# Performance work log

Measured on AMD Instinct MI355X. Metric: run time of the kernel, lower is better.

Reference implementation:

```python
import jax, jax.numpy as jnp
import numpy as np

B, D, H = 16384, 1024, 8
DH = D // H
LN_EPS = 1e-5


def setup_inputs() -> dict:
    key = jax.random.key(0)
    ks = jax.random.split(key, 16)
    s = 0.02  # weight init scale to keep softmax logits sane
    d = {}
    d['f40'] = jax.random.normal(ks[0], (B, D), jnp.float32)
    d['f100'] = jax.random.normal(ks[1], (B, D), jnp.float32)
    d['f200'] = jax.random.normal(ks[2], (B, D), jnp.float32)
    d['f400'] = jax.random.normal(ks[3], (B, D), jnp.float32)
    d['mag_emb'] = jax.random.normal(ks[4], (4, D), jnp.float32)
    i = 5
    for mag in ('100', '200', '400'):
        d[f'in_w_{mag}'] = jax.random.normal(ks[i], (3 * D, D), jnp.float32) * s
        d[f'in_b_{mag}'] = jnp.zeros((3 * D,), jnp.float32)
        d[f'out_w_{mag}'] = jax.random.normal(ks[i + 1], (D, D), jnp.float32) * s
        d[f'out_b_{mag}'] = jnp.zeros((D,), jnp.float32)
        d[f'ln_w_{mag}'] = jnp.ones((D,), jnp.float32)
        d[f'ln_b_{mag}'] = jnp.zeros((D,), jnp.float32)
        i += 2
    return d


def _layer_norm(x, w, b):
    m = jnp.mean(x, axis=-1, keepdims=True)
    v = jnp.mean(jnp.square(x - m), axis=-1, keepdims=True)
    return (x - m) * jax.lax.rsqrt(v + LN_EPS) * w + b


def _mha(q, kv, in_w, in_b, out_w, out_b):
    # q: [B,1,D], kv: [B,S,D]. Matches torch nn.MultiheadAttention (batch_first).
    S = kv.shape[1]
    wq, wk, wv = jnp.split(in_w, 3, axis=0)
    bq, bk, bv = jnp.split(in_b, 3)
    qp = (q @ wq.T + bq).reshape(B, 1, H, DH)
    kp = (kv @ wk.T + bk).reshape(B, S, H, DH)
    vp = (kv @ wv.T + bv).reshape(B, S, H, DH)
    scores = jnp.einsum('bqhd,bkhd->bhqk', qp, kp) / np.sqrt(DH).astype(np.float32)
    attn = jax.nn.softmax(scores, axis=-1)           # [B,H,1,S]
    out = jnp.einsum('bhqk,bkhd->bqhd', attn, vp).reshape(B, 1, D)
    out = (out @ out_w.T + out_b)[:, 0, :]           # [B,D]
    return out, attn.mean(axis=1)                     # weights averaged over heads: [B,1,S]


def reference(f40, f100, f200, f400, mag_emb,
              in_w_100, in_b_100, out_w_100, out_b_100, ln_w_100, ln_b_100,
              in_w_200, in_b_200, out_w_200, out_b_200, ln_w_200, ln_b_200,
              in_w_400, in_b_400, out_w_400, out_b_400, ln_w_400, ln_b_400):
    feats = (f40, f100, f200, f400)
    enh = [f + mag_emb[i] for i, f in enumerate(feats)]
    level_params = [
        (in_w_100, in_b_100, out_w_100, out_b_100, ln_w_100, ln_b_100),
        (in_w_200, in_b_200, out_w_200, out_b_200, ln_w_200, ln_b_200),
        (in_w_400, in_b_400, out_w_400, out_b_400, ln_w_400, ln_b_400),
    ]
    hier = [enh[0]]
    attn_maps = []
    for i, (iw, ib, ow, ob, lw, lb) in enumerate(level_params):
        ctx = jnp.stack(hier, axis=1)                 # [B, i+1, D]
        attended, w = _mha(enh[i + 1][:, None, :], ctx, iw, ib, ow, ob)
        fused = _layer_norm(enh[i + 1] + attended, lw, lb)
        hier.append(fused)
        attn_maps.append(w)
    return (hier[0], hier[1], hier[2], hier[3], attn_maps[0], attn_maps[1], attn_maps[2])
```

## Files before the change

### kernel.cpp

```cpp
#include <hip/hip_runtime.h>

typedef unsigned short u16;
typedef unsigned int u32;

#define NB 16384
#define ND 1024
static constexpr size_t BD = (size_t)NB * ND;
static constexpr size_t DD = (size_t)ND * ND;

typedef __attribute__((ext_vector_type(8))) short s16x8;
typedef __attribute__((ext_vector_type(4))) float f32x4;

__device__ __forceinline__ u16 f2bf(float f) {
  union { float f; u32 u; } v; v.f = f;
  return (u16)((v.u + 0x7fffu + ((v.u >> 16) & 1u)) >> 16);
}
__device__ __forceinline__ float asf(u32 u) {
  union { u32 u; float f; } v; v.u = u; return v.f;
}
__device__ __forceinline__ uint2 pack4(float a, float b, float c, float d) {
  uint2 p;
  p.x = (u32)f2bf(a) | ((u32)f2bf(b) << 16);
  p.y = (u32)f2bf(c) | ((u32)f2bf(d) << 16);
  return p;
}
__device__ __forceinline__ void load16bf(const u16* p, float* o) {
  const uint4* q = (const uint4*)p;
  uint4 u0 = q[0], u1 = q[1];
  u32 w[8] = {u0.x, u0.y, u0.z, u0.w, u1.x, u1.y, u1.z, u1.w};
#pragma unroll
  for (int i = 0; i < 8; ++i) {
    o[2 * i]     = asf(w[i] << 16);
    o[2 * i + 1] = asf(w[i] & 0xffff0000u);
  }
}
__device__ __forceinline__ void store16bf(u16* p, const float* o) {
  uint4 u0, u1;
  u0.x = (u32)f2bf(o[0])  | ((u32)f2bf(o[1])  << 16);
  u0.y = (u32)f2bf(o[2])  | ((u32)f2bf(o[3])  << 16);
  u0.z = (u32)f2bf(o[4])  | ((u32)f2bf(o[5])  << 16);
  u0.w = (u32)f2bf(o[6])  | ((u32)f2bf(o[7])  << 16);
  u1.x = (u32)f2bf(o[8])  | ((u32)f2bf(o[9])  << 16);
  u1.y = (u32)f2bf(o[10]) | ((u32)f2bf(o[11]) << 16);
  u1.z = (u32)f2bf(o[12]) | ((u32)f2bf(o[13]) << 16);
  u1.w = (u32)f2bf(o[14]) | ((u32)f2bf(o[15]) << 16);
  ((uint4*)p)[0] = u0;
  ((uint4*)p)[1] = u1;
}

#define G2L(gp, lp) __builtin_amdgcn_global_load_lds( \
    (__attribute__((address_space(1))) void*)(void*)(gp), \
    (__attribute__((address_space(3))) void*)(lp), 16, 0, 0)

template<int BF16_OUT>
__device__ __forceinline__ void gemm_core(
    const u16* __restrict__ A, const u16* __restrict__ Bm,
    const float* __restrict__ bias, void* __restrict__ Cp,
    int N, int K, int ldc, int row0, int col0)
{
  __shared__ __align__(16) u16 lA[128 * 64];
  __shared__ __align__(16) u16 lB[128 * 64];
  const int tid  = threadIdx.x;
  const int wave = tid >> 6;
  const int lane = tid & 63;
  const int wm = (wave >> 1) * 64;
  const int wn = (wave & 1) * 64;
  const int fr = lane & 15;
  const int fq = lane >> 4;
  const int srow = tid >> 3;
  const int scol = ((tid & 7) ^ (srow & 7)) * 8;

  f32x4 acc[4][4];
#pragma unroll
  for (int i = 0; i < 4; ++i)
#pragma unroll
    for (int j = 0; j < 4; ++j) acc[i][j] = (f32x4){0.f, 0.f, 0.f, 0.f};

  const u16* Abase = A  + (size_t)(row0 + srow) * K + scol;
  const u16* Bbase = Bm + (size_t)(col0 + srow) * K + scol;
  u16* lAw = lA + wave * 512;
  u16* lBw = lB + wave * 512;
  const int rsw = (fr & 7) << 3;

  for (int kt = 0; kt < K; kt += 64) {
#pragma unroll
    for (int c = 0; c < 4; ++c) {
      G2L(Abase + (size_t)(c * 32) * K + kt, lAw + c * 2048);
      G2L(Bbase + (size_t)(c * 32) * K + kt, lBw + c * 2048);
    }
    __syncthreads();

#pragma unroll
    for (int kk = 0; kk < 2; ++kk) {
      s16x8 af[4], bfr[4];
#pragma unroll
      for (int i = 0; i < 4; ++i) {
        af[i]  = *(const s16x8*)&lA[(wm + i * 16 + fr) * 64 + ((kk * 32 + fq * 8) ^ rsw)];
        bfr[i] = *(const s16x8*)&lB[(wn + i * 16 + fr) * 64 + ((kk * 32 + fq * 8) ^ rsw)];
      }
#pragma unroll
      for (int i = 0; i < 4; ++i)
#pragma unroll
        for (int j = 0; j < 4; ++j)
          acc[i][j] = __builtin_amdgcn_mfma_f32_16x16x32_bf16(af[i], bfr[j], acc[i][j], 0, 0, 0);
    }
    __syncthreads();
  }

#pragma unroll
  for (int i = 0; i < 4; ++i) {
#pragma unroll
    for (int j = 0; j < 4; ++j) {
      const int col = col0 + wn + j * 16 + fr;
      const float bb = bias ? bias[col] : 0.f;
#pragma unroll
      for (int r = 0; r < 4; ++r) {
        const int row = row0 + wm + i * 16 + fq * 4 + r;
        const float v = acc[i][j][r] + bb;
        if (BF16_OUT) ((u16*)Cp)[(size_t)row * ldc + col] = f2bf(v);
        else          ((float*)Cp)[(size_t)row * ldc + col] = v;
      }
    }
  }
}

__device__ __forceinline__ void swz_rowcol(int* row0, int* col0) {
  const int nwg = gridDim.x * gridDim.y;
  int wgid = blockIdx.y * gridDim.x + blockIdx.x;
  wgid = (wgid & 7) * (nwg >> 3) + (wgid >> 3);
  *row0 = (wgid / gridDim.x) * 128;
  *col0 = (wgid % gridDim.x) * 128;
}

template<int BF16_OUT>
__global__ __launch_bounds__(256, 3) void gemm_bt(
    const u16* __restrict__ A, const u16* __restrict__ Bm,
    const float* __restrict__ bias, void* __restrict__ Cp,
    int N, int K, int ldc)
{
  int row0, col0;
  swz_rowcol(&row0, &col0);
  gemm_core<BF16_OUT>(A, Bm, bias, Cp, N, K, ldc, row0, col0);
}

struct Ptr3 { const u16* a0; const u16* a1; const u16* a2;
              u16* c0; u16* c1; u16* c2; };

__global__ __launch_bounds__(256, 3) void kv_gemm(
    Ptr3 p, const u16* __restrict__ Bm, int K)
{
  int row0, col0;
  swz_rowcol(&row0, &col0);
  const u16* A; u16* C;
  if (blockIdx.z == 0)      { A = p.a0; C = p.c0; }
  else if (blockIdx.z == 1) { A = p.a1; C = p.c1; }
  else                      { A = p.a2; C = p.c2; }
  gemm_core<1>(A, Bm, nullptr, C, 2048, K, 2048, row0, col0);
}

__global__ __launch_bounds__(256) void prep_k(
    const float* __restrict__ f40, const float* __restrict__ f200,
    const float* __restrict__ f400, const float* __restrict__ mag,
    float* __restrict__ out0, u16* __restrict__ h0b,
    u16* __restrict__ e2b, u16* __restrict__ e3b)
{
  const size_t j = ((size_t)blockIdx.x * 256 + threadIdx.x) * 4;
  const int d = (int)(j & 1023);
  float4 m0 = *(const float4*)(mag + d);
  float4 m2 = *(const float4*)(mag + 2 * ND + d);
  float4 m3 = *(const float4*)(mag + 3 * ND + d);
  float4 a  = *(const float4*)(f40 + j);
  float4 c2 = *(const float4*)(f200 + j);
  float4 c3 = *(const float4*)(f400 + j);
  float4 h0;
  h0.x = a.x + m0.x; h0.y = a.y + m0.y; h0.z = a.z + m0.z; h0.w = a.w + m0.w;
  *(float4*)(out0 + j) = h0;
  *(uint2*)(h0b + j) = pack4(h0.x, h0.y, h0.z, h0.w);
  *(uint2*)(e2b + j) = pack4(c2.x + m2.x, c2.y + m2.y, c2.z + m2.z, c2.w + m2.w);
  *(uint2*)(e3b + j) = pack4(c3.x + m3.x, c3.y + m3.y, c3.z + m3.z, c3.w + m3.w);
}

__global__ __launch_bounds__(256) void ones_k(float* __restrict__ p) {
  p[blockIdx.x * 256 + threadIdx.x] = 1.0f;
}

__global__ __launch_bounds__(256) void convw_k(
    const float* __restrict__ iw, const float* __restrict__ ow,
    u16* __restrict__ wbf)
{
  const size_t j = ((size_t)blockIdx.x * 256 + threadIdx.x) * 4;
  const size_t IW = (size_t)3 * ND * ND;
  const float* src = (j < IW) ? (iw + j) : (ow + (j - IW));
  float4 v = *(const float4*)src;
  *(uint2*)(wbf + j) = pack4(v.x, v.y, v.z, v.w);
}

__global__ __launch_bounds__(256) void transpose_bf_k(
    const float* __restrict__ src, u16* __restrict__ dst)
{
  __shared__ float t[32][33];
  const int bx = blockIdx.x & 31, by = blockIdx.x >> 5;
  const int tx = threadIdx.x & 31, ty = threadIdx.x >> 5;
#pragma unroll
  for (int r = 0; r < 4; ++r)
    t[ty + r * 8][tx] = src[(size_t)(by * 32 + ty + r * 8) * ND + bx * 32 + tx];
  __syncthreads();
#pragma unroll
  for (int r = 0; r < 4; ++r)
    dst[(size_t)(bx * 32 + ty + r * 8) * ND + by * 32 + tx] = f2bf(t[tx][ty + r * 8]);
}

__global__ __launch_bounds__(256) void biasfold_k(
    const float* __restrict__ bv, const float* __restrict__ wo,
    const float* __restrict__ bo, float* __restrict__ c0)
{
  const int i = blockIdx.x;
  float s = 0.f;
  for (int k = threadIdx.x; k < ND; k += 256) s += bv[k] * wo[(size_t)i * ND + k];
#pragma unroll
  for (int m = 1; m <= 32; m <<= 1) s += __shfl_xor(s, m, 64);
  __shared__ float red[4];
  const int wv = threadIdx.x >> 6, ln = threadIdx.x & 63;
  if (ln == 0) red[wv] = s;
  __syncthreads();
  if (threadIdx.x == 0) c0[i] = bo[i] + red[0] + red[1] + red[2] + red[3];
}

template<int S>
__global__ __launch_bounds__(256) void attn_k(
    const u16* __restrict__ qp, const u16* __restrict__ kva,
    const u16* __restrict__ kvb, const u16* __restrict__ kvc,
    u16* __restrict__ att, float* __restrict__ amap)
{
  const int wave = threadIdx.x >> 6, lane = threadIdx.x & 63;
  const int b = blockIdx.x * 4 + wave;
  const int d0 = lane * 16;
  const u16* kv[3] = {kva, kvb, kvc};

  float q[16];
  load16bf(qp + (size_t)b * ND + d0, q);

  float sc[S];
  float mx = -1e30f;
#pragma unroll
  for (int s = 0; s < S; ++s) {
    float k[16];
    load16bf(kv[s] + (size_t)b * 2 * ND + d0, k);
    float dot = 0.f;
#pragma unroll
    for (int i = 0; i < 16; ++i) dot += q[i] * k[i];
    dot += __shfl_xor(dot, 1, 64);
    dot += __shfl_xor(dot, 2, 64);
    dot += __shfl_xor(dot, 4, 64);
    sc[s] = dot * 0.08838834764831845f;
    mx = fmaxf(mx, sc[s]);
  }
  float w_[S];
  float den = 0.f;
#pragma unroll
  for (int s = 0; s < S; ++s) { w_[s] = __expf(sc[s] - mx); den += w_[s]; }
  const float inv = 1.f / den;

  float o[16] = {0.f, 0.f, 0.f, 0.f, 0.f, 0.f, 0.f, 0.f,
                 0.f, 0.f, 0.f, 0.f, 0.f, 0.f, 0.f, 0.f};
#pragma unroll
  for (int s = 0; s < S; ++s) {
    float v[16];
    load16bf(kv[s] + (size_t)b * 2 * ND + ND + d0, v);
    const float ws = w_[s] * inv;
#pragma unroll
    for (int i = 0; i < 16; ++i) o[i] += ws * v[i];
  }
  store16bf(att + (size_t)b * ND + d0, o);

#pragma unroll
  for (int s = 0; s < S; ++s) {
    float t = w_[s] * inv;
    t += __shfl_xor(t, 8, 64);
    t += __shfl_xor(t, 16, 64);
    t += __shfl_xor(t, 32, 64);
    if (lane == 0) amap[(size_t)b * S + s] = t * 0.125f;
  }
}

__global__ __launch_bounds__(256) void ln_k(
    const float* __restrict__ f, const float* __restrict__ emb,
    const u16* __restrict__ ob, const float* __restrict__ lw,
    const float* __restrict__ lb, float* __restrict__ outp,
    u16* __restrict__ hbf)
{
  const int b = blockIdx.x, t = threadIdx.x;
  const int d = t * 4;
  const size_t off = (size_t)b * ND + d;
  float4 xf = *(const float4*)(f + off);
  float4 ef = *(const float4*)(emb + d);
  uint2 ov  = *(const uint2*)(ob + off);
  float o0 = asf(ov.x << 16), o1 = asf(ov.x & 0xffff0000u);
  float o2 = asf(ov.y << 16), o3 = asf(ov.y & 0xffff0000u);
  float x0 = xf.x + ef.x + o0;
  float x1 = xf.y + ef.y + o1;
  float x2 = xf.z + ef.z + o2;
  float x3 = xf.w + ef.w + o3;
  float s  = x0 + x1 + x2 + x3;
  float s2 = x0 * x0 + x1 * x1 + x2 * x2 + x3 * x3;
#pragma unroll
  for (int m = 1; m <= 32; m <<= 1) {
    s  += __shfl_xor(s,  m, 64);
    s2 += __shfl_xor(s2, m, 64);
  }
  __shared__ float red[8];
  const int wv = t >> 6, ln = t & 63;
  if (ln == 0) { red[wv] = s; red[4 + wv] = s2; }
  __syncthreads();
  s  = red[0] + red[1] + red[2] + red[3];
  s2 = red[4] + red[5] + red[6] + red[7];
  const float mean = s * (1.f / 1024.f);
  const float var  = s2 * (1.f / 1024.f) - mean * mean;
  const float r = rsqrtf(var + 1e-5f);
  float4 w4 = *(const float4*)(lw + d);
  float4 b4 = *(const float4*)(lb + d);
  float4 y;
  y.x = (x0 - mean) * r * w4.x + b4.x;
  y.y = (x1 - mean) * r * w4.y + b4.y;
  y.z = (x2 - mean) * r * w4.z + b4.z;
  y.w = (x3 - mean) * r * w4.w + b4.w;
  *(float4*)(outp + off) = y;
  if (hbf) *(uint2*)(hbf + off) = pack4(y.x, y.y, y.z, y.w);
}

extern "C" void kernel_launch(void* const* d_in, const int* in_sizes, int n_in,
                              void* d_out, int out_size, void* d_ws, size_t ws_size,
                              hipStream_t stream)
{
  const float* f40  = (const float*)d_in[0];
  const float* f100 = (const float*)d_in[1];
  const float* f200 = (const float*)d_in[2];
  const float* f400 = (const float*)d_in[3];
  const float* mag  = (const float*)d_in[4];
  const float* in_w[3]  = {(const float*)d_in[5],  (const float*)d_in[11], (const float*)d_in[17]};
  const float* in_b[3]  = {(const float*)d_in[6],  (const float*)d_in[12], (const float*)d_in[18]};
  const float* out_w[3] = {(const float*)d_in[7],  (const float*)d_in[13], (const float*)d_in[19]};
  const float* out_b[3] = {(const float*)d_in[8],  (const float*)d_in[14], (const float*)d_in[20]};
  const float* ln_w[3]  = {(const float*)d_in[9],  (const float*)d_in[15], (const float*)d_in[21]};
  const float* ln_b[3]  = {(const float*)d_in[10], (const float*)d_in[16], (const float*)d_in[22]};

  float* out = (float*)d_out;
  char* ws = (char*)d_ws;
  const size_t BF = BD * 2;
  u16* h0b  = (u16*)(ws);
  u16* h1b  = (u16*)(ws + BF);
  u16* h2b  = (u16*)(ws + 2 * BF);
  u16* qpb  = (u16*)(ws + 3 * BF);
  u16* attb = (u16*)(ws + 4 * BF);
  u16* kv0  = (u16*)(ws + 5 * BF);
  u16* kv1  = (u16*)(ws + 7 * BF);
  u16* kv2  = (u16*)(ws + 9 * BF);
  u16* wbf  = (u16*)(ws + 11 * BF);
  float* cs = (float*)(ws + 11 * BF + 8 * (1ull << 20));
  u16* e2b = kv1;
  u16* e3b = kv2;
  u16* hb[3] = {h0b, h1b, h2b};
  const float* f_lvl[3] = {f100, f200, f400};

  dim3 blk(256);
  prep_k<<<dim3((unsigned)(BD / 1024)), blk, 0, stream>>>(f40, f200, f400, mag, out, h0b, e2b, e3b);
  ones_k<<<dim3(NB / 256), blk, 0, stream>>>(out + 4 * BD);

  for (int l = 0; l < 3; ++l) {
    convw_k<<<dim3(4096), blk, 0, stream>>>(in_w[l], out_w[l], wbf);
    const u16* wq  = wbf;
    const u16* wkv = wbf + DD;
    const u16* wo  = wbf + 3 * DD;
    biasfold_k<<<dim3(1024), blk, 0, stream>>>(in_b[l] + 2 * ND, out_w[l], out_b[l], cs);

    if (l == 0) {
      u16* wvT = attb;
      u16* wvo = attb + DD;
      transpose_bf_k<<<dim3(1024), blk, 0, stream>>>(in_w[0] + 2 * DD, wvT);
      gemm_bt<1><<<dim3(8, 8), blk, 0, stream>>>(wo, wvT, nullptr, wvo, ND, ND, ND);
      gemm_bt<1><<<dim3(8, 128), blk, 0, stream>>>(h0b, wvo, cs, qpb, ND, ND, ND);
    } else {
      const u16* eb = (l == 1) ? e2b : e3b;
      gemm_bt<1><<<dim3(8, 128), blk, 0, stream>>>(eb, wq, in_b[l], qpb, ND, ND, ND);
      Ptr3 p = {hb[0], hb[1], hb[2], kv0, kv1, kv2};
      kv_gemm<<<dim3(16, 128, l + 1), blk, 0, stream>>>(p, wkv, ND);
      if (l == 1)
        attn_k<2><<<dim3(NB / 4), blk, 0, stream>>>(qpb, kv0, kv1, kv2, attb,
                                                    out + 4 * BD + NB);
      else
        attn_k<3><<<dim3(NB / 4), blk, 0, stream>>>(qpb, kv0, kv1, kv2, attb,
                                                    out + 4 * BD + 3 * NB);
      gemm_bt<1><<<dim3(8, 128), blk, 0, stream>>>(attb, wo, cs, qpb, ND, ND, ND);
    }
    ln_k<<<dim3(NB), blk, 0, stream>>>(f_lvl[l], mag + (size_t)(l + 1) * ND, qpb,
                                       ln_w[l], ln_b[l], out + (size_t)(l + 1) * BD,
                                       (l < 2) ? hb[l + 1] : nullptr);
  }
}
```

Measured before the change: 865.2 us.

## Mix context by attention weights before V projection instead of projecting every context row

Attention output is rewritten as sum_s w_s*(h_s Wv^T) = (sum_s w_s h_s) Wv^T per head. The key projection now covers only K (N=1024 instead of 2048). A score kernel writes per-head softmax weights, and a new av_gemm builds the weighted mix of the hidden states on the fly while loading A tiles, then runs a single V GEMM. This removes S-1 V projections per level at the cost of a software-loaded, non-async A path and bf16 rounding of the mixed input.

Measured after the change: 926.1 us. +7.0%, slower.

```diff
diff --git a/kernel.cpp b/kernel.cpp
--- a/kernel.cpp
+++ b/kernel.cpp
@@ -33,19 +33,6 @@
     o[2 * i]     = asf(w[i] << 16);
     o[2 * i + 1] = asf(w[i] & 0xffff0000u);
   }
-}
-__device__ __forceinline__ void store16bf(u16* p, const float* o) {
-  uint4 u0, u1;
-  u0.x = (u32)f2bf(o[0])  | ((u32)f2bf(o[1])  << 16);
-  u0.y = (u32)f2bf(o[2])  | ((u32)f2bf(o[3])  << 16);
-  u0.z = (u32)f2bf(o[4])  | ((u32)f2bf(o[5])  << 16);
-  u0.w = (u32)f2bf(o[6])  | ((u32)f2bf(o[7])  << 16);
-  u1.x = (u32)f2bf(o[8])  | ((u32)f2bf(o[9])  << 16);
-  u1.y = (u32)f2bf(o[10]) | ((u32)f2bf(o[11]) << 16);
-  u1.z = (u32)f2bf(o[12]) | ((u32)f2bf(o[13]) << 16);
-  u1.w = (u32)f2bf(o[14]) | ((u32)f2bf(o[15]) << 16);
-  ((uint4*)p)[0] = u0;
-  ((uint4*)p)[1] = u1;
 }
 
 #define G2L(gp, lp) __builtin_amdgcn_global_load_lds( \
@@ -124,12 +111,12 @@
   }
 }
 
-__device__ __forceinline__ void swz_rowcol(int* row0, int* col0) {
+__device__ __forceinline__ void swz_rowcol(int* row0, int* col0, int tile) {
   const int nwg = gridDim.x * gridDim.y;
   int wgid = blockIdx.y * gridDim.x + blockIdx.x;
   wgid = (wgid & 7) * (nwg >> 3) + (wgid >> 3);
-  *row0 = (wgid / gridDim.x) * 128;
-  *col0 = (wgid % gridDim.x) * 128;
+  *row0 = (wgid / gridDim.x) * tile;
+  *col0 = (wgid % gridDim.x) * tile;
 }
 
 template<int BF16_OUT>
@@ -139,23 +126,124 @@
     int N, int K, int ldc)
 {
   int row0, col0;
-  swz_rowcol(&row0, &col0);
+  swz_rowcol(&row0, &col0, 128);
   gemm_core<BF16_OUT>(A, Bm, bias, Cp, N, K, ldc, row0, col0);
 }
 
 struct Ptr3 { const u16* a0; const u16* a1; const u16* a2;
               u16* c0; u16* c1; u16* c2; };
 
-__global__ __launch_bounds__(256, 3) void kv_gemm(
+__global__ __launch_bounds__(256, 3) void kproj_gemm(
     Ptr3 p, const u16* __restrict__ Bm, int K)
 {
   int row0, col0;
-  swz_rowcol(&row0, &col0);
+  swz_rowcol(&row0, &col0, 128);
   const u16* A; u16* C;
   if (blockIdx.z == 0)      { A = p.a0; C = p.c0; }
   else if (blockIdx.z == 1) { A = p.a1; C = p.c1; }
   else                      { A = p.a2; C = p.c2; }
-  gemm_core<1>(A, Bm, nullptr, C, 2048, K, 2048, row0, col0);
+  gemm_core<1>(A, Bm, nullptr, C, 1024, K, 1024, row0, col0);
+}
+
+template<int S>
+__global__ __launch_bounds__(256, 3) void av_gemm(
+    const u16* __restrict__ hs0, const u16* __restrict__ hs1,
+    const u16* __restrict__ hs2, const float* __restrict__ wmix,
+    const u16* __restrict__ wv, u16* __restrict__ att)
+{
+  int row0, col0;
+  swz_rowcol(&row0, &col0, 128);
+  const int head = col0 >> 7;
+
+  __shared__ __align__(16) u16 lA[128 * 64];
+  __shared__ __align__(16) u16 lB[128 * 64];
+  const int tid  = threadIdx.x;
+  const int wave = tid >> 6;
+  const int lane = tid & 63;
+  const int wm = (wave >> 1) * 64;
+  const int wn = (wave & 1) * 64;
+  const int fr = lane & 15;
+  const int fq = lane >> 4;
+  const int srow = tid >> 3;
+  const int cg   = tid & 7;
+  const int scolB = (cg ^ (srow & 7)) * 8;
+  const int rsw = (fr & 7) << 3;
+
+  const u16* hsp[3] = {hs0, hs1, hs2};
+  float wr[4][S];
+#pragma unroll
+  for (int c = 0; c < 4; ++c) {
+    const int grow = row0 + c * 32 + srow;
+#pragma unroll
+    for (int s = 0; s < S; ++s)
+      wr[c][s] = wmix[((size_t)grow * 8 + head) * S + s];
+  }
+
+  f32x4 acc[4][4];
+#pragma unroll
+  for (int i = 0; i < 4; ++i)
+#pragma unroll
+    for (int j = 0; j < 4; ++j) acc[i][j] = (f32x4){0.f, 0.f, 0.f, 0.f};
+
+  const u16* Bbase = wv + (size_t)(col0 + srow) * ND + scolB;
+  u16* lBw = lB + wave * 512;
+
+  for (int kt = 0; kt < ND; kt += 64) {
+#pragma unroll
+    for (int c = 0; c < 4; ++c)
+      G2L(Bbase + (size_t)(c * 32) * ND + kt, lBw + c * 2048);
+#pragma unroll
+    for (int c = 0; c < 4; ++c) {
+      const int r = c * 32 + srow;
+      const size_t goff = (size_t)(row0 + r) * ND + kt + cg * 8;
+      float a8[8] = {0.f, 0.f, 0.f, 0.f, 0.f, 0.f, 0.f, 0.f};
+#pragma unroll
+      for (int s = 0; s < S; ++s) {
+        uint4 u = *(const uint4*)(hsp[s] + goff);
+        u32 wd[4] = {u.x, u.y, u.z, u.w};
+        const float ws = wr[c][s];
+#pragma unroll
+        for (int i = 0; i < 4; ++i) {
+          a8[2 * i]     += ws * asf(wd[i] << 16);
+          a8[2 * i + 1] += ws * asf(wd[i] & 0xffff0000u);
+        }
+      }
+      uint2 p0 = pack4(a8[0], a8[1], a8[2], a8[3]);
+      uint2 p1 = pack4(a8[4], a8[5], a8[6], a8[7]);
+      uint4 pv; pv.x = p0.x; pv.y = p0.y; pv.z = p1.x; pv.w = p1.y;
+      *(uint4*)&lA[r * 64 + ((cg ^ (r & 7)) * 8)] = pv;
+    }
+    __syncthreads();
+
+#pragma unroll
+    for (int kk = 0; kk < 2; ++kk) {
+      s16x8 af[4], bfr[4];
+#pragma unroll
+      for (int i = 0; i < 4; ++i) {
+        af[i]  = *(const s16x8*)&lA[(wm + i * 16 + fr) * 64 + ((kk * 32 + fq * 8) ^ rsw)];
+        bfr[i] = *(const s16x8*)&lB[(wn + i * 16 + fr) * 64 + ((kk * 32 + fq * 8) ^ rsw)];
+      }
+#pragma unroll
+      for (int i = 0; i < 4; ++i)
+#pragma unroll
+        for (int j = 0; j < 4; ++j)
+          acc[i][j] = __builtin_amdgcn_mfma_f32_16x16x32_bf16(af[i], bfr[j], acc[i][j], 0, 0, 0);
+    }
+    __syncthreads();
+  }
+
+#pragma unroll
+  for (int i = 0; i < 4; ++i) {
+#pragma unroll
+    for (int j = 0; j < 4; ++j) {
+      const int col = col0 + wn + j * 16 + fr;
+#pragma unroll
+      for (int r = 0; r < 4; ++r) {
+        const int row = row0 + wm + i * 16 + fq * 4 + r;
+        att[(size_t)row * ND + col] = f2bf(acc[i][j][r]);
+      }
+    }
+  }
 }
 
 __global__ __launch_bounds__(256) void prep_k(
@@ -227,15 +315,15 @@
 }
 
 template<int S>
-__global__ __launch_bounds__(256) void attn_k(
-    const u16* __restrict__ qp, const u16* __restrict__ kva,
-    const u16* __restrict__ kvb, const u16* __restrict__ kvc,
-    u16* __restrict__ att, float* __restrict__ amap)
+__global__ __launch_bounds__(256) void score_k(
+    const u16* __restrict__ qp, const u16* __restrict__ k0,
+    const u16* __restrict__ k1, const u16* __restrict__ k2,
+    float* __restrict__ wout, float* __restrict__ amap)
 {
   const int wave = threadIdx.x >> 6, lane = threadIdx.x & 63;
   const int b = blockIdx.x * 4 + wave;
   const int d0 = lane * 16;
-  const u16* kv[3] = {kva, kvb, kvc};
+  const u16* kp[3] = {k0, k1, k2};
 
   float q[16];
   load16bf(qp + (size_t)b * ND + d0, q);
@@ -245,7 +333,7 @@
 #pragma unroll
   for (int s = 0; s < S; ++s) {
     float k[16];
-    load16bf(kv[s] + (size_t)b * 2 * ND + d0, k);
+    load16bf(kp[s] + (size_t)b * ND + d0, k);
     float dot = 0.f;
 #pragma unroll
     for (int i = 0; i < 16; ++i) dot += q[i] * k[i];
@@ -261,21 +349,12 @@
   for (int s = 0; s < S; ++s) { w_[s] = __expf(sc[s] - mx); den += w_[s]; }
   const float inv = 1.f / den;
 
-  float o[16] = {0.f, 0.f, 0.f, 0.f, 0.f, 0.f, 0.f, 0.f,
-                 0.f, 0.f, 0.f, 0.f, 0.f, 0.f, 0.f, 0.f};
+  const int h = lane >> 3;
 #pragma unroll
   for (int s = 0; s < S; ++s) {
-    float v[16];
-    load16bf(kv[s] + (size_t)b * 2 * ND + ND + d0, v);
-    const float ws = w_[s] * inv;
-#pragma unroll
-    for (int i = 0; i < 16; ++i) o[i] += ws * v[i];
-  }
-  store16bf(att + (size_t)b * ND + d0, o);
-
-#pragma unroll
-  for (int s = 0; s < S; ++s) {
-    float t = w_[s] * inv;
+    const float wv_ = w_[s] * inv;
+    if ((lane & 7) == 0) wout[((size_t)b * 8 + h) * S + s] = wv_;
+    float t = wv_;
     t += __shfl_xor(t, 8, 64);
     t += __shfl_xor(t, 16, 64);
     t += __shfl_xor(t, 32, 64);
@@ -353,6 +432,7 @@
   u16* qpb  = (u16*)(ws + 3 * BF);
   u16* attb = (u16*)(ws + 4 * BF);
   u16* kv0  = (u16*)(ws + 5 * BF);
+  float* wmix = (float*)(ws + 6 * BF);
   u16* kv1  = (u16*)(ws + 7 * BF);
   u16* kv2  = (u16*)(ws + 9 * BF);
   u16* wbf  = (u16*)(ws + 11 * BF);
@@ -369,7 +449,8 @@
   for (int l = 0; l < 3; ++l) {
     convw_k<<<dim3(4096), blk, 0, stream>>>(in_w[l], out_w[l], wbf);
     const u16* wq  = wbf;
-    const u16* wkv = wbf + DD;
+    const u16* wk  = wbf + DD;
+    const u16* wvB = wbf + 2 * DD;
     const u16* wo  = wbf + 3 * DD;
     biasfold_k<<<dim3(1024), blk, 0, stream>>>(in_b[l] + 2 * ND, out_w[l], out_b[l], cs);
 
@@ -383,13 +464,16 @@
       const u16* eb = (l == 1) ? e2b : e3b;
       gemm_bt<1><<<dim3(8, 128), blk, 0, stream>>>(eb, wq, in_b[l], qpb, ND, ND, ND);
       Ptr3 p = {hb[0], hb[1], hb[2], kv0, kv1, kv2};
-      kv_gemm<<<dim3(16, 128, l + 1), blk, 0, stream>>>(p, wkv, ND);
-      if (l == 1)
-        attn_k<2><<<dim3(NB / 4), blk, 0, stream>>>(qpb, kv0, kv1, kv2, attb,
-                                                    out + 4 * BD + NB);
-      else
-        attn_k<3><<<dim3(NB / 4), blk, 0, stream>>>(qpb, kv0, kv1, kv2, attb,
-                                                    out + 4 * BD + 3 * NB);
+      kproj_gemm<<<dim3(8, 128, l + 1), blk, 0, stream>>>(p, wk, ND);
+      if (l == 1) {
+        score_k<2><<<dim3(NB / 4), blk, 0, stream>>>(qpb, kv0, kv1, kv2, wmix,
+                                                     out + 4 * BD + NB);
+        av_gemm<2><<<dim3(8, 128), blk, 0, stream>>>(h0b, h1b, h2b, wmix, wvB, attb);
+      } else {
+        score_k<3><<<dim3(NB / 4), blk, 0, stream>>>(qpb, kv0, kv1, kv2, wmix,
+                                                     out + 4 * BD + 3 * NB);
+        av_gemm<3><<<dim3(8, 128), blk, 0, stream>>>(h0b, h1b, h2b, wmix, wvB, attb);
+      }
       gemm_bt<1><<<dim3(8, 128), blk, 0, stream>>>(attb, wo, cs, qpb, ND, ND, ND);
     }
     ln_k<<<dim3(NB), blk, 0, stream>>>(f_lvl[l], mag + (size_t)(l + 1) * ND, qpb,
```
